# Kernel tuning notes

Measured on AMD Instinct MI355X. Metric: run time of the kernel, lower is better.

## Reference

```python
import jax, jax.numpy as jnp
import numpy as np

B, L, E, H, D, OUT = 4, 2048, 1024, 8, 128, 1024


def setup_inputs() -> dict:
    key = jax.random.key(0)
    ks = jax.random.split(key, 6)
    stdv = 1.0 / np.sqrt(D)
    return {
        "k": jax.random.normal(ks[0], (B, L, E), dtype=jnp.float32),
        "q": jax.random.normal(ks[1], (B, L, E), dtype=jnp.float32),
        "w_kx": jax.random.uniform(ks[2], (H, E, D), minval=-stdv, maxval=stdv, dtype=jnp.float32),
        "w_qx": jax.random.uniform(ks[3], (H, E, D), minval=-stdv, maxval=stdv, dtype=jnp.float32),
        "proj_w": jax.random.normal(ks[4], (OUT, H * D), dtype=jnp.float32) * 0.02,
        "proj_b": jnp.zeros((OUT,), dtype=jnp.float32),
        "flag": False,
    }


def reference(k, q, w_kx, w_qx, proj_w, proj_b, flag):
    # Per-head sigmoid projections, vectorized over heads (original loops over heads).
    d = w_kx.shape[-1]
    kx = jax.nn.sigmoid(jnp.einsum('ble,hed->bhld', k, w_kx))  # [B,H,Lk,D]
    if flag:
        # flag==True: q is used directly (already hidden_dim-sized), shared across heads
        qx = jnp.broadcast_to(q[:, None], (q.shape[0], kx.shape[1], q.shape[1], q.shape[2]))
    else:
        qx = jax.nn.sigmoid(jnp.einsum('bqe,hed->bhqd', q, w_qx))  # [B,H,Lq,D]
    # scaled dot-product score + softmax over key axis
    score = jnp.einsum('bhqd,bhkd->bhqk', qx, kx) * (1.0 / jnp.sqrt(jnp.asarray(d, kx.dtype)))
    attn = jax.nn.softmax(score, axis=-1)
    out = jnp.einsum('bhqk,bhkd->bhqd', attn, kx)  # [B,H,Lq,D]
    # concat heads along feature dim, then linear projection (dropout p=0 -> identity)
    b, h, lq, _ = out.shape
    out = out.transpose(0, 2, 1, 3).reshape(b, lq, h * d)
    return out @ proj_w.T + proj_b
```

## Files before the change

### kernel.cpp

```cpp
#include <hip/hip_runtime.h>

#define BB 4
#define LL 2048
#define EE 1024
#define HH 8
#define DD 128
#define OO 1024
#define MM (BB*LL)
#define ND (HH*DD)

#define QBLK 128
#define KVBLK 64
#define NT (LL / KVBLK)

#define C2 0.12751920678739807f

typedef __bf16 bf16;
typedef unsigned short u16;
typedef __bf16 bf16x8 __attribute__((ext_vector_type(8)));
typedef __bf16 bf16x4 __attribute__((ext_vector_type(4)));
typedef float  f32x4  __attribute__((ext_vector_type(4)));

__device__ __forceinline__ void gl16(const bf16* g, bf16* l) {
#if __has_builtin(__builtin_amdgcn_global_load_lds)
    __builtin_amdgcn_global_load_lds((const __attribute__((address_space(1))) char*)g,
                                     (__attribute__((address_space(3))) char*)l, 16, 0, 0);
#else
    *(bf16x8*)l = *(const bf16x8*)g;
#endif
}

__device__ __forceinline__ float fexp2(float x) {
#if __has_builtin(__builtin_amdgcn_exp2f)
    return __builtin_amdgcn_exp2f(x);
#else
    return exp2f(x);
#endif
}

__device__ __forceinline__ bf16x8 cvt8p(float4 f0, float4 f1) {
    bf16x8 v;
    v[0] = (bf16)f0.x; v[1] = (bf16)f0.y; v[2] = (bf16)f0.z; v[3] = (bf16)f0.w;
    v[4] = (bf16)f1.x; v[5] = (bf16)f1.y; v[6] = (bf16)f1.z; v[7] = (bf16)f1.w;
    return v;
}

__global__ void detect_kernel(const u16* __restrict__ data, int* __restrict__ mode) {
    const int l = threadIdx.x;
    int cnt = 0;
#pragma unroll
    for (int i = 0; i < 8; i++) {
        int e = (data[l * 8 + i] >> 7) & 0xFF;
        cnt += (e >= 117 && e <= 132) ? 1 : 0;
    }
    cnt += __shfl_xor(cnt, 1);
    cnt += __shfl_xor(cnt, 2);
    cnt += __shfl_xor(cnt, 4);
    cnt += __shfl_xor(cnt, 8);
    cnt += __shfl_xor(cnt, 16);
    cnt += __shfl_xor(cnt, 32);
    if (l == 0) *mode = (cnt > 400) ? 1 : 0;
}

__global__ __launch_bounds__(256) void fill_kernel(float* __restrict__ out, float v, int n) {
    int i = blockIdx.x * 256 + threadIdx.x;
    if (i < n) out[i] = v;
}

__global__ __launch_bounds__(256) void wtrans_kernel(const void* __restrict__ in0,
                                                     const void* __restrict__ in1,
                                                     bf16* __restrict__ outT0,
                                                     bf16* __restrict__ outT1,
                                                     const int* __restrict__ mode) {
    const void* in = blockIdx.y ? in1 : in0;
    bf16* outT = blockIdx.y ? outT1 : outT0;
    int idx = blockIdx.x * 256 + threadIdx.x;
    int i4 = idx * 4;
    int h = i4 >> 17;
    int rem = i4 & 131071;
    int e = rem >> 7;
    int d = rem & 127;
    size_t ob = ((size_t)h * DD + d) * EE + e;
    if (*mode) {
        bf16x4 v = *(const bf16x4*)((const bf16*)in + i4);
        outT[ob]          = v[0];
        outT[ob + EE]     = v[1];
        outT[ob + 2 * EE] = v[2];
        outT[ob + 3 * EE] = v[3];
    } else {
        float4 v = *(const float4*)((const float*)in + i4);
        outT[ob]          = (bf16)v.x;
        outT[ob + EE]     = (bf16)v.y;
        outT[ob + 2 * EE] = (bf16)v.z;
        outT[ob + 3 * EE] = (bf16)v.w;
    }
}

__global__ __launch_bounds__(256) void gemm_kernel(const void* __restrict__ A0,
                                                   const void* __restrict__ A1,
                                                   const void* __restrict__ BT0,
                                                   const void* __restrict__ BT1,
                                                   bf16* __restrict__ outBF0,
                                                   bf16* __restrict__ outBF1,
                                                   bf16* __restrict__ outT,
                                                   float* __restrict__ outF,
                                                   const void* __restrict__ PB,
                                                   const int* __restrict__ mode,
                                                   const int epi) {
    __shared__ __align__(16) bf16 As[128 * 64];
    __shared__ __align__(16) bf16 Bs[128 * 64];
    const int md = *mode;
    const int t = threadIdx.x;
    const int w = t >> 6, l = t & 63;
    const int lr = l & 15, lg = l >> 4;
    const int wr = w >> 1, wc = w & 1;
    const int o = blockIdx.x + (blockIdx.y << 3);
    const int half = (epi == 3) ? (o >> 9) : 0;
    const int oo = o & 511;
    const int mt = (oo & 7) * 8 + ((oo >> 3) & 7);
    const int ntile = oo >> 6;
    const int m0 = mt * 128, n0 = ntile * 128;
    const void* A = half ? A1 : A0;
    const void* BT = half ? BT1 : BT0;

    const int useF = (md == 0);
    const float* fS = (const float*)((epi == 3) ? A : BT);
    bf16* fDst = (epi == 3) ? As : Bs;
    const int f0 = (epi == 3) ? m0 : n0;
    const bf16* gS = (const bf16*)((epi == 3) ? BT : A);
    bf16* gDst = (epi == 3) ? Bs : As;
    const int g0 = (epi == 3) ? n0 : m0;

    f32x4 acc[4][4];
    const f32x4 zero = {0.f, 0.f, 0.f, 0.f};
#pragma unroll
    for (int i = 0; i < 4; i++)
#pragma unroll
        for (int j = 0; j < 4; j++) acc[i][j] = zero;

    float4 rS[4][2];
    if (useF) {
#pragma unroll
        for (int p = 0; p < 4; p++) {
            const int id = p * 256 + t;
            const int row = id >> 3, cc = id & 7;
            const float* src = fS + (size_t)(f0 + row) * 1024 + cc * 8;
            rS[p][0] = *(const float4*)src;
            rS[p][1] = *(const float4*)(src + 4);
        }
    }

    for (int kt = 0; kt < 16; ++kt) {
        const int k0 = kt * 64;
        __syncthreads();
        if (useF) {
#pragma unroll
            for (int p = 0; p < 4; p++) {
                const int id = p * 256 + t;
                const int row = id >> 3, cc = id & 7;
                *(bf16x8*)(fDst + row * 64 + ((cc ^ (row & 7)) << 3)) = cvt8p(rS[p][0], rS[p][1]);
            }
#pragma unroll
            for (int p = 0; p < 4; p++) {
                const int id = p * 256 + t;
                const int row = id >> 3;
                const int c = (id & 7) ^ (row & 7);
                gl16(gS + (size_t)(g0 + row) * 1024 + k0 + c * 8, gDst + (p * 256 + w * 64) * 8);
            }
        } else {
#pragma unroll
            for (int p = 0; p < 4; p++) {
                const int id = p * 256 + t;
                const int row = id >> 3;
                const int c = (id & 7) ^ (row & 7);
                gl16((const bf16*)A + (size_t)(m0 + row) * 1024 + k0 + c * 8,
                     As + (p * 256 + w * 64) * 8);
                gl16((const bf16*)BT + (size_t)(n0 + row) * 1024 + k0 + c * 8,
                     Bs + (p * 256 + w * 64) * 8);
            }
        }
        __syncthreads();
        if (useF && kt + 1 < 16) {
            const int k0n = k0 + 64;
#pragma unroll
            for (int p = 0; p < 4; p++) {
                const int id = p * 256 + t;
                const int row = id >> 3, cc = id & 7;
                const float* src = fS + (size_t)(f0 + row) * 1024 + k0n + cc * 8;
                rS[p][0] = *(const float4*)src;
                rS[p][1] = *(const float4*)(src + 4);
            }
        }
        bf16x8 af[4][2], bg[4][2];
#pragma unroll
        for (int i = 0; i < 4; i++) {
            const int ar = wr * 64 + i * 16 + lr;
#pragma unroll
            for (int ks = 0; ks < 2; ks++)
                af[i][ks] = *(const bf16x8*)(As + ar * 64 + (((ks * 4 + lg) ^ (ar & 7)) << 3));
        }
#pragma unroll
        for (int j = 0; j < 4; j++) {
            const int br = wc * 64 + j * 16 + lr;
#pragma unroll
            for (int ks = 0; ks < 2; ks++)
                bg[j][ks] = *(const bf16x8*)(Bs + br * 64 + (((ks * 4 + lg) ^ (br & 7)) << 3));
        }
#pragma unroll
        for (int i = 0; i < 4; i++)
#pragma unroll
            for (int j = 0; j < 4; j++) {
                acc[i][j] = __builtin_amdgcn_mfma_f32_16x16x32_bf16(af[i][0], bg[j][0], acc[i][j], 0, 0, 0);
                acc[i][j] = __builtin_amdgcn_mfma_f32_16x16x32_bf16(af[i][1], bg[j][1], acc[i][j], 0, 0, 0);
            }
    }

    if (epi == 3) {
        bf16* outBF = half ? outBF1 : outBF0;
        const float mulf = half ? C2 : 1.0f;
        const int b_idx = m0 >> 11;
        const int h = n0 >> 7;
#pragma unroll
        for (int i = 0; i < 4; i++) {
#pragma unroll
            for (int j = 0; j < 4; j++) {
                const int gr = m0 + wr * 64 + i * 16 + lg * 4;
                const int gc = n0 + wc * 64 + j * 16 + lr;
                float s0 = mulf / (1.0f + __expf(-acc[i][j][0]));
                float s1 = mulf / (1.0f + __expf(-acc[i][j][1]));
                float s2 = mulf / (1.0f + __expf(-acc[i][j][2]));
                float s3 = mulf / (1.0f + __expf(-acc[i][j][3]));
                outBF[(size_t)gr * ND + gc]           = (bf16)s0;
                outBF[(size_t)(gr + 1) * ND + gc]     = (bf16)s1;
                outBF[(size_t)(gr + 2) * ND + gc]     = (bf16)s2;
                outBF[(size_t)(gr + 3) * ND + gc]     = (bf16)s3;
                if (!half) {
                    bf16x4 pk;
                    pk[0] = (bf16)s0; pk[1] = (bf16)s1; pk[2] = (bf16)s2; pk[3] = (bf16)s3;
                    const int d = gc & 127;
                    const int lrow = gr & 2047;
                    *(bf16x4*)(outT + (((size_t)(h * BB + b_idx)) * DD + d) * LL + lrow) = pk;
                }
            }
        }
    } else {
#pragma unroll
        for (int j = 0; j < 4; j++) {
            const int gc = n0 + wc * 64 + j * 16 + lr;
            const float bias = md ? (float)((const bf16*)PB)[gc] : ((const float*)PB)[gc];
#pragma unroll
            for (int i = 0; i < 4; i++) {
                const int gr = m0 + wr * 64 + i * 16 + lg * 4;
#pragma unroll
                for (int reg = 0; reg < 4; reg++)
                    outF[(size_t)(gr + reg) * OO + gc] = acc[i][j][reg] + bias;
            }
        }
    }
}

__global__ __launch_bounds__(512, 4) void attn_kernel(const bf16* __restrict__ QX,
                                                      const bf16* __restrict__ KX,
                                                      const bf16* __restrict__ KXT,
                                                      bf16* __restrict__ AO) {
    __shared__ __align__(16) bf16 Kl[2][KVBLK * 128];
    __shared__ __align__(16) bf16 Vt[2][128 * KVBLK];
    __shared__ __align__(16) bf16 Pl[8][16 * 64];
    const int t = threadIdx.x;
    const int w = t >> 6, l = t & 63;
    const int lr = l & 15, lg = l >> 4;
    const int bid = blockIdx.x;
    const int orig = (bid & 7) * 64 + (bid >> 3);
    const int bh = orig >> 4;
    const int h = bh & 7, b = bh >> 3;
    const int q0 = (orig & 15) * QBLK;
    const bf16* qxh = QX + (size_t)(b * LL) * ND + h * DD;
    const bf16* kxh = KX + (size_t)(b * LL) * ND + h * DD;
    const bf16* kxt = KXT + ((size_t)(h * BB + b)) * DD * LL;

    const int kid1 = 512 + t;
    const int krow0 = t >> 4,    kcc0 = t & 15;
    const int krow1 = kid1 >> 4, kcc1 = kid1 & 15;
    const int vrow0 = t >> 3,    vcc0 = t & 7;
    const int vrow1 = kid1 >> 3, vcc1 = kid1 & 7;
    const bf16* kp0 = kxh + (size_t)krow0 * ND + kcc0 * 8;
    const bf16* kp1 = kxh + (size_t)krow1 * ND + kcc1 * 8;
    const bf16* vp0 = kxt + (size_t)vrow0 * LL + vcc0 * 8;
    const bf16* vp1 = kxt + (size_t)vrow1 * LL + vcc1 * 8;
    const int kw0 = krow0 * 128 + ((kcc0 ^ (krow0 & 15)) << 3);
    const int kw1 = krow1 * 128 + ((kcc1 ^ (krow1 & 15)) << 3);
    const int vw0 = vrow0 * 64 + ((vcc0 ^ (vrow0 & 7)) << 3);
    const int vw1 = vrow1 * 64 + ((vcc1 ^ (vrow1 & 7)) << 3);

    bf16x8 qf[4];
    const int qrow = q0 + w * 16 + lr;
#pragma unroll
    for (int s = 0; s < 4; s++)
        qf[s] = *(const bf16x8*)(qxh + (size_t)qrow * ND + s * 32 + lg * 8);

    bf16x8 rk0 = *(const bf16x8*)(kp0);
    bf16x8 rk1 = *(const bf16x8*)(kp1);
    bf16x8 rv0 = *(const bf16x8*)(vp0);
    bf16x8 rv1 = *(const bf16x8*)(vp1);
    *(bf16x8*)(Kl[0] + kw0) = rk0;
    *(bf16x8*)(Kl[0] + kw1) = rk1;
    *(bf16x8*)(Vt[0] + vw0) = rv0;
    *(bf16x8*)(Vt[0] + vw1) = rv1;
    rk0 = *(const bf16x8*)(kp0 + (size_t)KVBLK * ND);
    rk1 = *(const bf16x8*)(kp1 + (size_t)KVBLK * ND);
    rv0 = *(const bf16x8*)(vp0 + KVBLK);
    rv1 = *(const bf16x8*)(vp1 + KVBLK);
    __syncthreads();

    f32x4 oacc[8];
    const f32x4 zero = {0.f, 0.f, 0.f, 0.f};
#pragma unroll
    for (int n = 0; n < 8; n++) oacc[n] = zero;
    float psum = 0.f;

    for (int kt = 0; kt < NT; ++kt) {
        const int cur = kt & 1;
        if (kt + 1 < NT) {
            *(bf16x8*)(Kl[cur ^ 1] + kw0) = rk0;
            *(bf16x8*)(Kl[cur ^ 1] + kw1) = rk1;
            *(bf16x8*)(Vt[cur ^ 1] + vw0) = rv0;
            *(bf16x8*)(Vt[cur ^ 1] + vw1) = rv1;
            if (kt + 2 < NT) {
                const size_t ko = (size_t)(kt + 2) * KVBLK * ND;
                const int vo = (kt + 2) * KVBLK;
                rk0 = *(const bf16x8*)(kp0 + ko);
                rk1 = *(const bf16x8*)(kp1 + ko);
                rv0 = *(const bf16x8*)(vp0 + vo);
                rv1 = *(const bf16x8*)(vp1 + vo);
            }
        }
        const bf16* KlC = Kl[cur];
        const bf16* VtC = Vt[cur];

        f32x4 sa[4];
        __builtin_amdgcn_s_setprio(1);
#pragma unroll
        for (int n = 0; n < 2; n++) {
            sa[n] = zero;
#pragma unroll
            for (int ks = 0; ks < 4; ks++) {
                int arow = n * 16 + lr;
                bf16x8 kb = *(const bf16x8*)(KlC + arow * 128 + ((((ks * 4 + lg) ^ (arow & 15))) << 3));
                sa[n] = __builtin_amdgcn_mfma_f32_16x16x32_bf16(kb, qf[ks], sa[n], 0, 0, 0);
            }
        }
        __builtin_amdgcn_s_setprio(0);
#pragma unroll
        for (int n = 0; n < 2; n++) {
            bf16x4 pk;
#pragma unroll
            for (int j = 0; j < 4; j++) {
                float p = fexp2(sa[n][j]);
                psum += p;
                pk[j] = (bf16)p;
            }
            const int chunk = (2 * n + (lg >> 1)) ^ (lr & 7);
            *(bf16x4*)(Pl[w] + lr * 64 + chunk * 8 + (lg & 1) * 4) = pk;
        }
        __builtin_amdgcn_s_setprio(1);
#pragma unroll
        for (int n = 2; n < 4; n++) {
            sa[n] = zero;
#pragma unroll
            for (int ks = 0; ks < 4; ks++) {
                int arow = n * 16 + lr;
                bf16x8 kb = *(const bf16x8*)(KlC + arow * 128 + ((((ks * 4 + lg) ^ (arow & 15))) << 3));
                sa[n] = __builtin_amdgcn_mfma_f32_16x16x32_bf16(kb, qf[ks], sa[n], 0, 0, 0);
            }
        }
        __builtin_amdgcn_s_setprio(0);
#pragma unroll
        for (int n = 2; n < 4; n++) {
            bf16x4 pk;
#pragma unroll
            for (int j = 0; j < 4; j++) {
                float p = fexp2(sa[n][j]);
                psum += p;
                pk[j] = (bf16)p;
            }
            const int chunk = (2 * n + (lg >> 1)) ^ (lr & 7);
            *(bf16x4*)(Pl[w] + lr * 64 + chunk * 8 + (lg & 1) * 4) = pk;
        }
        asm volatile("s_waitcnt lgkmcnt(0)" ::: "memory");
        __builtin_amdgcn_sched_barrier(0);
        bf16x8 pb0 = *(const bf16x8*)(Pl[w] + lr * 64 + (((lg ^ (lr & 7))) << 3));
        bf16x8 pb1 = *(const bf16x8*)(Pl[w] + lr * 64 + ((((4 + lg) ^ (lr & 7))) << 3));
        __builtin_amdgcn_s_setprio(1);
#pragma unroll
        for (int n = 0; n < 8; n++) {
            int vrow = n * 16 + lr;
            bf16x8 vb0 = *(const bf16x8*)(VtC + vrow * 64 + (((lg ^ (vrow & 7))) << 3));
            oacc[n] = __builtin_amdgcn_mfma_f32_16x16x32_bf16(vb0, pb0, oacc[n], 0, 0, 0);
            bf16x8 vb1 = *(const bf16x8*)(VtC + vrow * 64 + ((((4 + lg) ^ (vrow & 7))) << 3));
            oacc[n] = __builtin_amdgcn_mfma_f32_16x16x32_bf16(vb1, pb1, oacc[n], 0, 0, 0);
        }
        __builtin_amdgcn_s_setprio(0);
        __syncthreads();
    }
    float tot = psum;
    tot += __shfl_xor(tot, 16);
    tot += __shfl_xor(tot, 32);
    const float linv = 1.0f / tot;
    const int arow = b * LL + q0 + w * 16 + lr;
    bf16* aoRow = AO + (size_t)arow * ND + h * DD;
#pragma unroll
    for (int n = 0; n < 8; n++) {
        bf16x4 o;
#pragma unroll
        for (int reg = 0; reg < 4; reg++) o[reg] = (bf16)(oacc[n][reg] * linv);
        *(bf16x4*)(aoRow + n * 16 + lg * 4) = o;
    }
}

extern "C" void kernel_launch(void* const* d_in, const int* in_sizes, int n_in,
                              void* d_out, int out_size, void* d_ws, size_t ws_size,
                              hipStream_t stream) {
    (void)in_sizes; (void)n_in;
    float* out = (float*)d_out;

    const size_t NEED = ((size_t)(2 + 2 + 16 + 16 + 16 + 16) << 20) + 256;
    if (ws_size < NEED) {
        hipLaunchKernelGGL(fill_kernel, dim3((out_size + 255) / 256), dim3(256), 0, stream,
                           out, (float)(ws_size >> 20), out_size);
        return;
    }

    int* mode = (int*)d_ws;
    bf16* base = (bf16*)((char*)d_ws + 256);
    bf16* wkT = base;
    bf16* wqT = wkT + (size_t)HH * DD * EE;
    bf16* kx  = wqT + (size_t)HH * DD * EE;
    bf16* qx  = kx  + (size_t)MM * ND;
    bf16* kxT = qx  + (size_t)MM * ND;
    bf16* ao  = kxT + (size_t)HH * MM * DD;

    hipLaunchKernelGGL(detect_kernel, dim3(1), dim3(64), 0, stream, (const u16*)d_in[0], mode);
    hipLaunchKernelGGL(wtrans_kernel, dim3(HH * EE * DD / 4 / 256, 2), dim3(256), 0, stream,
                       d_in[2], d_in[3], wkT, wqT, mode);
    hipLaunchKernelGGL(gemm_kernel, dim3(8, 128), dim3(256), 0, stream,
                       d_in[0], d_in[1], wkT, wqT, kx, qx, kxT,
                       (float*)nullptr, (const void*)nullptr, mode, 3);
    hipLaunchKernelGGL(attn_kernel, dim3(512), dim3(512), 0, stream, qx, kx, kxT, ao);
    hipLaunchKernelGGL(gemm_kernel, dim3(8, 64), dim3(256), 0, stream,
                       ao, (const void*)nullptr, d_in[4], (const void*)nullptr,
                       (bf16*)nullptr, (bf16*)nullptr, (bf16*)nullptr, out, d_in[5], mode, 2);
}
```

Measured before the change: 175.6 us.

## Halve attention tile sizes to 64 queries and 32 keys per block

Shrinks the attention kernel's query tile to 64 rows (4 waves) and KV tile to 32 keys, doubling the grid to 1024 blocks of 256 threads. LDS swizzles, the P staging layout and the PV MFMA loop are reworked for the smaller tiles. The aim is more blocks for better load balance and occupancy, at the cost of twice the K/V reloads per query and twice as many barrier-separated iterations.

```diff
diff --git a/kernel.cpp b/kernel.cpp
--- a/kernel.cpp
+++ b/kernel.cpp
@@ -9,8 +9,8 @@
 #define MM (BB*LL)
 #define ND (HH*DD)
 
-#define QBLK 128
-#define KVBLK 64
+#define QBLK 64
+#define KVBLK 32
 #define NT (LL / KVBLK)
 
 #define C2 0.12751920678739807f
@@ -259,38 +259,38 @@
     }
 }
 
-__global__ __launch_bounds__(512, 4) void attn_kernel(const bf16* __restrict__ QX,
+__global__ __launch_bounds__(256, 4) void attn_kernel(const bf16* __restrict__ QX,
                                                       const bf16* __restrict__ KX,
                                                       const bf16* __restrict__ KXT,
                                                       bf16* __restrict__ AO) {
-    __shared__ __align__(16) bf16 Kl[2][KVBLK * 128];
-    __shared__ __align__(16) bf16 Vt[2][128 * KVBLK];
-    __shared__ __align__(16) bf16 Pl[8][16 * 64];
+    __shared__ __align__(16) bf16 Kl[2 * KVBLK * 128];
+    __shared__ __align__(16) bf16 Vt[2 * 128 * KVBLK];
+    __shared__ __align__(16) bf16 Pl[4][16 * KVBLK];
     const int t = threadIdx.x;
     const int w = t >> 6, l = t & 63;
     const int lr = l & 15, lg = l >> 4;
     const int bid = blockIdx.x;
-    const int orig = (bid & 7) * 64 + (bid >> 3);
-    const int bh = orig >> 4;
+    const int orig = (bid & 7) * 128 + (bid >> 3);
+    const int bh = orig >> 5;
     const int h = bh & 7, b = bh >> 3;
-    const int q0 = (orig & 15) * QBLK;
+    const int q0 = (orig & 31) * QBLK;
     const bf16* qxh = QX + (size_t)(b * LL) * ND + h * DD;
     const bf16* kxh = KX + (size_t)(b * LL) * ND + h * DD;
     const bf16* kxt = KXT + ((size_t)(h * BB + b)) * DD * LL;
 
-    const int kid1 = 512 + t;
+    const int kid1 = 256 + t;
     const int krow0 = t >> 4,    kcc0 = t & 15;
     const int krow1 = kid1 >> 4, kcc1 = kid1 & 15;
-    const int vrow0 = t >> 3,    vcc0 = t & 7;
-    const int vrow1 = kid1 >> 3, vcc1 = kid1 & 7;
+    const int vrow0 = t >> 2,    vcc0 = t & 3;
+    const int vrow1 = kid1 >> 2, vcc1 = kid1 & 3;
     const bf16* kp0 = kxh + (size_t)krow0 * ND + kcc0 * 8;
     const bf16* kp1 = kxh + (size_t)krow1 * ND + kcc1 * 8;
     const bf16* vp0 = kxt + (size_t)vrow0 * LL + vcc0 * 8;
     const bf16* vp1 = kxt + (size_t)vrow1 * LL + vcc1 * 8;
     const int kw0 = krow0 * 128 + ((kcc0 ^ (krow0 & 15)) << 3);
     const int kw1 = krow1 * 128 + ((kcc1 ^ (krow1 & 15)) << 3);
-    const int vw0 = vrow0 * 64 + ((vcc0 ^ (vrow0 & 7)) << 3);
-    const int vw1 = vrow1 * 64 + ((vcc1 ^ (vrow1 & 7)) << 3);
+    const int vw0 = vrow0 * 32 + ((vcc0 ^ (vrow0 & 3)) << 3);
+    const int vw1 = vrow1 * 32 + ((vcc1 ^ (vrow1 & 3)) << 3);
 
     bf16x8 qf[4];
     const int qrow = q0 + w * 16 + lr;
@@ -302,10 +302,10 @@
     bf16x8 rk1 = *(const bf16x8*)(kp1);
     bf16x8 rv0 = *(const bf16x8*)(vp0);
     bf16x8 rv1 = *(const bf16x8*)(vp1);
-    *(bf16x8*)(Kl[0] + kw0) = rk0;
-    *(bf16x8*)(Kl[0] + kw1) = rk1;
-    *(bf16x8*)(Vt[0] + vw0) = rv0;
-    *(bf16x8*)(Vt[0] + vw1) = rv1;
+    *(bf16x8*)(Kl + kw0) = rk0;
+    *(bf16x8*)(Kl + kw1) = rk1;
+    *(bf16x8*)(Vt + vw0) = rv0;
+    *(bf16x8*)(Vt + vw1) = rv1;
     rk0 = *(const bf16x8*)(kp0 + (size_t)KVBLK * ND);
     rk1 = *(const bf16x8*)(kp1 + (size_t)KVBLK * ND);
     rv0 = *(const bf16x8*)(vp0 + KVBLK);
@@ -320,11 +320,13 @@
 
     for (int kt = 0; kt < NT; ++kt) {
         const int cur = kt & 1;
+        const int co = cur * 4096;
         if (kt + 1 < NT) {
-            *(bf16x8*)(Kl[cur ^ 1] + kw0) = rk0;
-            *(bf16x8*)(Kl[cur ^ 1] + kw1) = rk1;
-            *(bf16x8*)(Vt[cur ^ 1] + vw0) = rv0;
-            *(bf16x8*)(Vt[cur ^ 1] + vw1) = rv1;
+            const int ao = (cur ^ 1) * 4096;
+            *(bf16x8*)(Kl + ao + kw0) = rk0;
+            *(bf16x8*)(Kl + ao + kw1) = rk1;
+            *(bf16x8*)(Vt + ao + vw0) = rv0;
+            *(bf16x8*)(Vt + ao + vw1) = rv1;
             if (kt + 2 < NT) {
                 const size_t ko = (size_t)(kt + 2) * KVBLK * ND;
                 const int vo = (kt + 2) * KVBLK;
@@ -334,70 +336,56 @@
                 rv1 = *(const bf16x8*)(vp1 + vo);
             }
         }
-        const bf16* KlC = Kl[cur];
-        const bf16* VtC = Vt[cur];
-
-        f32x4 sa[4];
+        const bf16* KlC = Kl + co;
+        const bf16* VtC = Vt + co;
+
+        f32x4 sa[2];
         __builtin_amdgcn_s_setprio(1);
-#pragma unroll
-        for (int n = 0; n < 2; n++) {
-            sa[n] = zero;
-#pragma unroll
-            for (int ks = 0; ks < 4; ks++) {
-                int arow = n * 16 + lr;
-                bf16x8 kb = *(const bf16x8*)(KlC + arow * 128 + ((((ks * 4 + lg) ^ (arow & 15))) << 3));
-                sa[n] = __builtin_amdgcn_mfma_f32_16x16x32_bf16(kb, qf[ks], sa[n], 0, 0, 0);
-            }
+        sa[0] = zero;
+#pragma unroll
+        for (int ks = 0; ks < 4; ks++) {
+            bf16x8 kb = *(const bf16x8*)(KlC + lr * 128 + ((((ks * 4 + lg) ^ lr)) << 3));
+            sa[0] = __builtin_amdgcn_mfma_f32_16x16x32_bf16(kb, qf[ks], sa[0], 0, 0, 0);
         }
         __builtin_amdgcn_s_setprio(0);
-#pragma unroll
-        for (int n = 0; n < 2; n++) {
+        {
             bf16x4 pk;
 #pragma unroll
             for (int j = 0; j < 4; j++) {
-                float p = fexp2(sa[n][j]);
+                float p = fexp2(sa[0][j]);
                 psum += p;
                 pk[j] = (bf16)p;
             }
-            const int chunk = (2 * n + (lg >> 1)) ^ (lr & 7);
-            *(bf16x4*)(Pl[w] + lr * 64 + chunk * 8 + (lg & 1) * 4) = pk;
+            const int phys = lg ^ (lr & 6);
+            *(bf16x4*)(Pl[w] + lr * 32 + phys * 4) = pk;
         }
         __builtin_amdgcn_s_setprio(1);
-#pragma unroll
-        for (int n = 2; n < 4; n++) {
-            sa[n] = zero;
-#pragma unroll
-            for (int ks = 0; ks < 4; ks++) {
-                int arow = n * 16 + lr;
-                bf16x8 kb = *(const bf16x8*)(KlC + arow * 128 + ((((ks * 4 + lg) ^ (arow & 15))) << 3));
-                sa[n] = __builtin_amdgcn_mfma_f32_16x16x32_bf16(kb, qf[ks], sa[n], 0, 0, 0);
-            }
+        sa[1] = zero;
+#pragma unroll
+        for (int ks = 0; ks < 4; ks++) {
+            bf16x8 kb = *(const bf16x8*)(KlC + 2048 + lr * 128 + ((((ks * 4 + lg) ^ lr)) << 3));
+            sa[1] = __builtin_amdgcn_mfma_f32_16x16x32_bf16(kb, qf[ks], sa[1], 0, 0, 0);
         }
         __builtin_amdgcn_s_setprio(0);
-#pragma unroll
-        for (int n = 2; n < 4; n++) {
+        {
             bf16x4 pk;
 #pragma unroll
             for (int j = 0; j < 4; j++) {
-                float p = fexp2(sa[n][j]);
+                float p = fexp2(sa[1][j]);
                 psum += p;
                 pk[j] = (bf16)p;
             }
-            const int chunk = (2 * n + (lg >> 1)) ^ (lr & 7);
-            *(bf16x4*)(Pl[w] + lr * 64 + chunk * 8 + (lg & 1) * 4) = pk;
+            const int phys = (4 + lg) ^ (lr & 6);
+            *(bf16x4*)(Pl[w] + lr * 32 + phys * 4) = pk;
         }
         asm volatile("s_waitcnt lgkmcnt(0)" ::: "memory");
         __builtin_amdgcn_sched_barrier(0);
-        bf16x8 pb0 = *(const bf16x8*)(Pl[w] + lr * 64 + (((lg ^ (lr & 7))) << 3));
-        bf16x8 pb1 = *(const bf16x8*)(Pl[w] + lr * 64 + ((((4 + lg) ^ (lr & 7))) << 3));
+        bf16x8 pb = *(const bf16x8*)(Pl[w] + lr * 32 + (((2 * lg) ^ (lr & 6)) << 2));
         __builtin_amdgcn_s_setprio(1);
 #pragma unroll
         for (int n = 0; n < 8; n++) {
-            int vrow = n * 16 + lr;
-            bf16x8 vb0 = *(const bf16x8*)(VtC + vrow * 64 + (((lg ^ (vrow & 7))) << 3));
-            oacc[n] = __builtin_amdgcn_mfma_f32_16x16x32_bf16(vb0, pb0, oacc[n], 0, 0, 0);
-            bf16x8 vb1 = *(const bf16x8*)(VtC + vrow * 64 + ((((4 + lg) ^ (vrow & 7))) << 3));
-            oacc[n] = __builtin_amdgcn_mfma_f32_16x16x32_bf16(vb1, pb1, oacc[n], 0, 0, 0);
+            bf16x8 vb = *(const bf16x8*)(VtC + n * 512 + lr * 32 + (((lg ^ (lr & 3))) << 3));
+            oacc[n] = __builtin_amdgcn_mfma_f32_16x16x32_bf16(vb, pb, oacc[n], 0, 0, 0);
         }
         __builtin_amdgcn_s_setprio(0);
         __syncthreads();
@@ -445,7 +433,7 @@
     hipLaunchKernelGGL(gemm_kernel, dim3(8, 128), dim3(256), 0, stream,
                        d_in[0], d_in[1], wkT, wqT, kx, qx, kxT,
                        (float*)nullptr, (const void*)nullptr, mode, 3);
-    hipLaunchKernelGGL(attn_kernel, dim3(512), dim3(512), 0, stream, qx, kx, kxT, ao);
+    hipLaunchKernelGGL(attn_kernel, dim3(1024), dim3(256), 0, stream, qx, kx, kxT, ao);
     hipLaunchKernelGGL(gemm_kernel, dim3(8, 64), dim3(256), 0, stream,
                        ao, (const void*)nullptr, d_in[4], (const void*)nullptr,
                        (bf16*)nullptr, (bf16*)nullptr, (bf16*)nullptr, out, d_in[5], mode, 2);
```

Measured after the change: 191.8 us. +9.2%, slower.
